# Performance work log

Measured on AMD Instinct MI355X. Metric: run time of the kernel, lower is better.

Reference implementation:

```python
import jax, jax.numpy as jnp
import numpy as np

N_NODES = 100000

def _graph_conv(x, src, dst, W, b, num_nodes):
    # DGL GraphConv, norm='both', edge_weight=None:
    # h = D_in^{-1/2} * A * (D_out^{-1/2} * x @ W) + b
    ones = jnp.ones(src.shape[0], dtype=x.dtype)
    out_deg = jax.ops.segment_sum(ones, src, num_segments=num_nodes)
    in_deg = jax.ops.segment_sum(ones, dst, num_segments=num_nodes)
    norm_src = jax.lax.rsqrt(jnp.clip(out_deg, 1.0))  # [N]
    norm_dst = jax.lax.rsqrt(jnp.clip(in_deg, 1.0))   # [N]
    h = (x * norm_src[:, None]) @ W                    # [N, out] (weight first: in>=out)
    msg = h[src]                                       # gather over edges [E, out]
    agg = jax.ops.segment_sum(msg, dst, num_segments=num_nodes)  # scatter-add [N, out]
    return agg * norm_dst[:, None] + b


def setup_inputs() -> dict:
    key = jax.random.key(0)
    k = jax.random.split(key, 8)
    N, F, H, C, E = N_NODES, 512, 16, 40, 3200000
    x = jax.random.normal(k[0], (N, F), dtype=jnp.float32)
    edge_src = jax.random.randint(k[1], (E,), 0, N, dtype=jnp.int32)
    edge_dst = jax.random.randint(k[2], (E,), 0, N, dtype=jnp.int32)
    # Glorot-style init for GraphConv weights, zero bias (DGL defaults)
    W1 = jax.random.normal(k[3], (F, H), dtype=jnp.float32) * (1.0 / np.sqrt(F))
    b1 = jnp.zeros((H,), dtype=jnp.float32)
    W2 = jax.random.normal(k[4], (H, C), dtype=jnp.float32) * (1.0 / np.sqrt(H))
    b2 = jnp.zeros((C,), dtype=jnp.float32)
    return {"x": x, "edge_src": edge_src, "edge_dst": edge_dst,
            "W1": W1, "b1": b1, "W2": W2, "b2": b2}


def reference(x, edge_src, edge_dst, W1, b1, W2, b2):
    h = _graph_conv(x, edge_src, edge_dst, W1, b1, N_NODES)
    h = jax.nn.relu(h)
    # dropout p=0.5 is identity in eval mode
    out = _graph_conv(h, edge_src, edge_dst, W2, b2, N_NODES)
    return out
```

## Files before the change

kernel.cpp:

```cpp
#include <hip/hip_runtime.h>

#define F_IN  512
#define H_DIM 16
#define C_OUT 40
#define NBLK_P 256

static inline size_t align_up(size_t x, size_t a) { return (x + a - 1) / a * a; }

__global__ __launch_bounds__(256) void k_pcount(const int* __restrict__ keys, int E,
        int chunk, int nbk, int* __restrict__ histT) {
    __shared__ int h[512];
    for (int i = threadIdx.x; i < nbk; i += 256) h[i] = 0;
    __syncthreads();
    int b = blockIdx.x;
    int s = b * chunk, e = min(s + chunk, E);
    for (int i = s + threadIdx.x; i < e; i += 256)
        atomicAdd(&h[keys[i] >> 8], 1);
    __syncthreads();
    for (int i = threadIdx.x; i < nbk; i += 256)
        histT[i * NBLK_P + b] = h[i];
}

__global__ void k_scan1(const int* __restrict__ in, int* __restrict__ out,
                        int* __restrict__ bsums, int n) {
    __shared__ int tmp[256];
    int t = threadIdx.x;
    int gid = blockIdx.x * 256 + t;
    int v = (gid < n) ? in[gid] : 0;
    tmp[t] = v;
    __syncthreads();
    for (int off = 1; off < 256; off <<= 1) {
        int add = (t >= off) ? tmp[t - off] : 0;
        __syncthreads();
        tmp[t] += add;
        __syncthreads();
    }
    if (gid < n) out[gid] = tmp[t] - v;
    if (t == 255) bsums[blockIdx.x] = tmp[255];
}

__global__ void k_scan2(int* bsums, int nb) {
    __shared__ int tmp[512];
    int t = threadIdx.x;
    int v = (t < nb) ? bsums[t] : 0;
    tmp[t] = v;
    __syncthreads();
    for (int off = 1; off < 512; off <<= 1) {
        int add = (t >= off) ? tmp[t - off] : 0;
        __syncthreads();
        tmp[t] += add;
        __syncthreads();
    }
    if (t < nb) bsums[t] = tmp[t] - v;
}

__global__ void k_scan3(int* __restrict__ out, const int* __restrict__ bsums, int n) {
    int gid = blockIdx.x * 256 + threadIdx.x;
    if (gid < n) out[gid] += bsums[blockIdx.x];
}

__global__ __launch_bounds__(256) void k_pscat_key(const int* __restrict__ keys, int E,
        int chunk, const int* __restrict__ histT, int* __restrict__ outk) {
    __shared__ int cnt[512];
    for (int i = threadIdx.x; i < 512; i += 256) cnt[i] = 0;
    __syncthreads();
    int b = blockIdx.x;
    int s = b * chunk, e = min(s + chunk, E);
    for (int i = s + threadIdx.x; i < e; i += 256) {
        int k = keys[i];
        int bk = k >> 8;
        int r = atomicAdd(&cnt[bk], 1);
        outk[histT[bk * NBLK_P + b] + r] = k;
    }
}

__global__ __launch_bounds__(256) void k_pscat_pair(const int* __restrict__ src,
        const int* __restrict__ dst, int E, int chunk,
        const int* __restrict__ histT, int2* __restrict__ outp) {
    __shared__ int cnt[512];
    for (int i = threadIdx.x; i < 512; i += 256) cnt[i] = 0;
    __syncthreads();
    int b = blockIdx.x;
    int s = b * chunk, e = min(s + chunk, E);
    for (int i = s + threadIdx.x; i < e; i += 256) {
        int d = dst[i];
        int bk = d >> 8;
        int r = atomicAdd(&cnt[bk], 1);
        outp[histT[bk * NBLK_P + b] + r] = make_int2(src[i], d);
    }
}

__global__ __launch_bounds__(256) void k_bcount(const int* __restrict__ keysb,
        const int* __restrict__ histT, int nbk, int E, int N, int* __restrict__ deg) {
    __shared__ int h[256];
    int t = threadIdx.x, b = blockIdx.x;
    int bstart = histT[b * NBLK_P];
    int bend = (b + 1 < nbk) ? histT[(b + 1) * NBLK_P] : E;
    h[t] = 0;
    __syncthreads();
    for (int i = bstart + t; i < bend; i += 256)
        atomicAdd(&h[keysb[i] & 255], 1);
    __syncthreads();
    int node = (b << 8) + t;
    if (node < N) deg[node] = h[t];
}

__global__ __launch_bounds__(256) void k_bbuild(const int2* __restrict__ pairsb,
        const int* __restrict__ histT, int nbk, int E, int N,
        int* __restrict__ indeg, int* __restrict__ csroff, int* __restrict__ csrsrc) {
    __shared__ int h[256], offs[256], cnt[256], tmp[256];
    int t = threadIdx.x, b = blockIdx.x;
    int bstart = histT[b * NBLK_P];
    int bend = (b + 1 < nbk) ? histT[(b + 1) * NBLK_P] : E;
    h[t] = 0; cnt[t] = 0;
    __syncthreads();
    for (int i = bstart + t; i < bend; i += 256)
        atomicAdd(&h[pairsb[i].y & 255], 1);
    __syncthreads();
    int v = h[t];
    tmp[t] = v;
    __syncthreads();
    for (int off = 1; off < 256; off <<= 1) {
        int add = (t >= off) ? tmp[t - off] : 0;
        __syncthreads();
        tmp[t] += add;
        __syncthreads();
    }
    offs[t] = tmp[t] - v;
    __syncthreads();
    int node = (b << 8) + t;
    if (node < N) {
        indeg[node] = v;
        csroff[node] = bstart + offs[t];
    }
    for (int i = bstart + t; i < bend; i += 256) {
        int2 p = pairsb[i];
        int l = p.y & 255;
        int r = atomicAdd(&cnt[l], 1);
        csrsrc[bstart + offs[l] + r] = p.x;
    }
}

__global__ __launch_bounds__(256) void k_gemm1(const float* __restrict__ x,
        const float* __restrict__ W1, const int* __restrict__ outdeg,
        float* __restrict__ h1, int n) {
    __shared__ float Ws[F_IN * H_DIM];
    for (int i = threadIdx.x; i < F_IN * H_DIM / 4; i += 256)
        ((float4*)Ws)[i] = ((const float4*)W1)[i];
    __syncthreads();

    int row = blockIdx.x * 256 + threadIdx.x;
    if (row >= n) return;
    const float4* xr = (const float4*)(x + (size_t)row * F_IN);

    float acc[H_DIM];
#pragma unroll
    for (int j = 0; j < H_DIM; ++j) acc[j] = 0.f;

    for (int c = 0; c < F_IN / 16; ++c) {
        float4 xv0 = xr[c * 4 + 0];
        float4 xv1 = xr[c * 4 + 1];
        float4 xv2 = xr[c * 4 + 2];
        float4 xv3 = xr[c * 4 + 3];
        float xs[16] = {xv0.x, xv0.y, xv0.z, xv0.w,
                        xv1.x, xv1.y, xv1.z, xv1.w,
                        xv2.x, xv2.y, xv2.z, xv2.w,
                        xv3.x, xv3.y, xv3.z, xv3.w};
#pragma unroll
        for (int kk = 0; kk < 16; ++kk) {
            const float* wr = &Ws[(c * 16 + kk) * H_DIM];
#pragma unroll
            for (int j = 0; j < H_DIM; ++j) acc[j] += xs[kk] * wr[j];
        }
    }

    float ns = rsqrtf(fmaxf((float)outdeg[row], 1.f));
    float4* o = (float4*)(h1 + (size_t)row * H_DIM);
#pragma unroll
    for (int qq = 0; qq < 4; ++qq)
        o[qq] = make_float4(acc[qq * 4 + 0] * ns, acc[qq * 4 + 1] * ns,
                            acc[qq * 4 + 2] * ns, acc[qq * 4 + 3] * ns);
}

__global__ __launch_bounds__(256) void k_agg1(const int* __restrict__ csroff,
        const int* __restrict__ indeg, const int* __restrict__ outdeg,
        const int* __restrict__ csrsrc, const float* __restrict__ h1,
        const float* __restrict__ b1, float* __restrict__ g, int n) {
    int t = threadIdx.x;
    int q = t & 3;
    int lv = t >> 2;
    int v = blockIdx.x * 64 + lv;
    if (v >= n) return;
    int start = csroff[v];
    int len = indeg[v];
    const float4* h4 = (const float4*)h1;
    float4 acc = make_float4(0.f, 0.f, 0.f, 0.f);
    for (int i = 0; i < len; ++i) {
        int s = csrsrc[start + i];
        float4 m = h4[(size_t)s * 4 + q];
        acc.x += m.x; acc.y += m.y; acc.z += m.z; acc.w += m.w;
    }
    float nd = rsqrtf(fmaxf((float)len, 1.f));
    float ns = rsqrtf(fmaxf((float)outdeg[v], 1.f));
    float4 bb = ((const float4*)b1)[q];
    float4 r;
    r.x = fmaxf(acc.x * nd + bb.x, 0.f) * ns;
    r.y = fmaxf(acc.y * nd + bb.y, 0.f) * ns;
    r.z = fmaxf(acc.z * nd + bb.z, 0.f) * ns;
    r.w = fmaxf(acc.w * nd + bb.w, 0.f) * ns;
    ((float4*)g)[(size_t)v * 4 + q] = r;
}

__global__ __launch_bounds__(256) void k_agg2(const int* __restrict__ csroff,
        const int* __restrict__ indeg, const int* __restrict__ csrsrc,
        const float* __restrict__ gbuf, const float* __restrict__ W2,
        const float* __restrict__ b2, float* __restrict__ out, int n) {
    __shared__ float Ws[H_DIM * C_OUT];
    __shared__ float agg[64][17];
    int t = threadIdx.x;
    for (int i = t; i < H_DIM * C_OUT; i += 256) Ws[i] = W2[i];

    int q = t & 3;
    int lv = t >> 2;
    int v = blockIdx.x * 64 + lv;
    float4 acc = make_float4(0.f, 0.f, 0.f, 0.f);
    if (v < n) {
        int start = csroff[v];
        int len = indeg[v];
        const float4* g4 = (const float4*)gbuf;
        for (int i = 0; i < len; ++i) {
            int s = csrsrc[start + i];
            float4 m = g4[(size_t)s * 4 + q];
            acc.x += m.x; acc.y += m.y; acc.z += m.z; acc.w += m.w;
        }
    }
    agg[lv][q * 4 + 0] = acc.x;
    agg[lv][q * 4 + 1] = acc.y;
    agg[lv][q * 4 + 2] = acc.z;
    agg[lv][q * 4 + 3] = acc.w;
    __syncthreads();

    for (int idx = t; idx < 64 * C_OUT; idx += 256) {
        int dlv = idx / C_OUT;
        int c = idx % C_OUT;
        int dv = blockIdx.x * 64 + dlv;
        if (dv < n) {
            float s = 0.f;
#pragma unroll
            for (int k = 0; k < H_DIM; ++k) s += agg[dlv][k] * Ws[k * C_OUT + c];
            float nd = rsqrtf(fmaxf((float)indeg[dv], 1.f));
            out[(size_t)dv * C_OUT + c] = s * nd + b2[c];
        }
    }
}

extern "C" void kernel_launch(void* const* d_in, const int* in_sizes, int n_in,
                              void* d_out, int out_size, void* d_ws, size_t ws_size,
                              hipStream_t stream) {
    const float* x  = (const float*)d_in[0];
    const int* esrc = (const int*)d_in[1];
    const int* edst = (const int*)d_in[2];
    const float* W1 = (const float*)d_in[3];
    const float* b1 = (const float*)d_in[4];
    const float* W2 = (const float*)d_in[5];
    const float* b2 = (const float*)d_in[6];
    float* out = (float*)d_out;

    const int N = in_sizes[0] / F_IN;
    const int E = in_sizes[1];
    const int nbk = (N + 255) >> 8;
    const int n2 = nbk * NBLK_P;
    const int chunk = (E + NBLK_P - 1) / NBLK_P;

    char* p = (char*)d_ws;
    auto alloc = [&](size_t bytes) -> char* {
        char* r = p; p += align_up(bytes, 256); return r;
    };
    int*  histS  = (int*)alloc((size_t)n2 * 4);
    int*  histT  = (int*)alloc((size_t)n2 * 4);
    int*  bsums  = (int*)alloc(512 * 4);
    int2* pairsb = (int2*)alloc((size_t)E * 8);
    int*  srcb   = (int*)alloc((size_t)E * 4);
    int*  indeg  = (int*)alloc((size_t)N * 4);
    int*  outdeg = (int*)alloc((size_t)N * 4);
    int*  csroff = (int*)alloc((size_t)N * 4);

    int*   csrsrc = srcb;
    float* h1     = (float*)pairsb;
    float* g      = h1 + (size_t)N * H_DIM;

    int nbs = (n2 + 255) / 256;

    k_pcount<<<NBLK_P, 256, 0, stream>>>(esrc, E, chunk, nbk, histS);
    k_scan1<<<nbs, 256, 0, stream>>>(histS, histS, bsums, n2);
    k_scan2<<<1, 512, 0, stream>>>(bsums, nbs);
    k_scan3<<<nbs, 256, 0, stream>>>(histS, bsums, n2);
    k_pscat_key<<<NBLK_P, 256, 0, stream>>>(esrc, E, chunk, histS, srcb);
    k_bcount<<<nbk, 256, 0, stream>>>(srcb, histS, nbk, E, N, outdeg);

    k_pcount<<<NBLK_P, 256, 0, stream>>>(edst, E, chunk, nbk, histT);
    k_scan1<<<nbs, 256, 0, stream>>>(histT, histT, bsums, n2);
    k_scan2<<<1, 512, 0, stream>>>(bsums, nbs);
    k_scan3<<<nbs, 256, 0, stream>>>(histT, bsums, n2);
    k_pscat_pair<<<NBLK_P, 256, 0, stream>>>(esrc, edst, E, chunk, histT, pairsb);
    k_bbuild<<<nbk, 256, 0, stream>>>(pairsb, histT, nbk, E, N, indeg, csroff, csrsrc);

    k_gemm1<<<(N + 255) / 256, 256, 0, stream>>>(x, W1, outdeg, h1, N);
    int nb64 = (N + 63) / 64;
    k_agg1<<<nb64, 256, 0, stream>>>(csroff, indeg, outdeg, csrsrc, h1, b1, g, N);
    k_agg2<<<nb64, 256, 0, stream>>>(csroff, indeg, csrsrc, g, W2, b2, out, N);
}
```

Before: 316.1 us.

## Fuse src/dst CSR build passes and pack bucketed edges into compact formats

```diff
diff --git a/kernel.cpp b/kernel.cpp
--- a/kernel.cpp
+++ b/kernel.cpp
@@ -7,115 +7,115 @@
 
 static inline size_t align_up(size_t x, size_t a) { return (x + a - 1) / a * a; }
 
-__global__ __launch_bounds__(256) void k_pcount(const int* __restrict__ keys, int E,
-        int chunk, int nbk, int* __restrict__ histT) {
-    __shared__ int h[512];
-    for (int i = threadIdx.x; i < nbk; i += 256) h[i] = 0;
-    __syncthreads();
-    int b = blockIdx.x;
-    int s = b * chunk, e = min(s + chunk, E);
-    for (int i = s + threadIdx.x; i < e; i += 256)
-        atomicAdd(&h[keys[i] >> 8], 1);
-    __syncthreads();
-    for (int i = threadIdx.x; i < nbk; i += 256)
-        histT[i * NBLK_P + b] = h[i];
-}
-
-__global__ void k_scan1(const int* __restrict__ in, int* __restrict__ out,
-                        int* __restrict__ bsums, int n) {
-    __shared__ int tmp[256];
-    int t = threadIdx.x;
-    int gid = blockIdx.x * 256 + t;
-    int v = (gid < n) ? in[gid] : 0;
-    tmp[t] = v;
-    __syncthreads();
-    for (int off = 1; off < 256; off <<= 1) {
-        int add = (t >= off) ? tmp[t - off] : 0;
-        __syncthreads();
-        tmp[t] += add;
-        __syncthreads();
-    }
-    if (gid < n) out[gid] = tmp[t] - v;
-    if (t == 255) bsums[blockIdx.x] = tmp[255];
-}
-
-__global__ void k_scan2(int* bsums, int nb) {
-    __shared__ int tmp[512];
-    int t = threadIdx.x;
-    int v = (t < nb) ? bsums[t] : 0;
-    tmp[t] = v;
-    __syncthreads();
-    for (int off = 1; off < 512; off <<= 1) {
-        int add = (t >= off) ? tmp[t - off] : 0;
-        __syncthreads();
-        tmp[t] += add;
-        __syncthreads();
-    }
-    if (t < nb) bsums[t] = tmp[t] - v;
-}
-
-__global__ void k_scan3(int* __restrict__ out, const int* __restrict__ bsums, int n) {
-    int gid = blockIdx.x * 256 + threadIdx.x;
-    if (gid < n) out[gid] += bsums[blockIdx.x];
-}
-
-__global__ __launch_bounds__(256) void k_pscat_key(const int* __restrict__ keys, int E,
-        int chunk, const int* __restrict__ histT, int* __restrict__ outk) {
-    __shared__ int cnt[512];
-    for (int i = threadIdx.x; i < 512; i += 256) cnt[i] = 0;
+__global__ __launch_bounds__(256) void k_pcount(const int* __restrict__ src,
+        const int* __restrict__ dst, int E, int chunk, int nbk,
+        int* __restrict__ histS, int* __restrict__ histT) {
+    __shared__ int hs[512], hd[512];
+    for (int i = threadIdx.x; i < 512; i += 256) { hs[i] = 0; hd[i] = 0; }
     __syncthreads();
     int b = blockIdx.x;
     int s = b * chunk, e = min(s + chunk, E);
     for (int i = s + threadIdx.x; i < e; i += 256) {
-        int k = keys[i];
-        int bk = k >> 8;
-        int r = atomicAdd(&cnt[bk], 1);
-        outk[histT[bk * NBLK_P + b] + r] = k;
-    }
-}
-
-__global__ __launch_bounds__(256) void k_pscat_pair(const int* __restrict__ src,
+        atomicAdd(&hs[src[i] >> 8], 1);
+        atomicAdd(&hd[dst[i] >> 8], 1);
+    }
+    __syncthreads();
+    for (int i = threadIdx.x; i < nbk; i += 256) {
+        histS[i * NBLK_P + b] = hs[i];
+        histT[i * NBLK_P + b] = hd[i];
+    }
+}
+
+__global__ void k_scan1(int* __restrict__ histS, int* __restrict__ histT,
+                        int* __restrict__ bsums) {
+    __shared__ int tmp[256];
+    int* h = blockIdx.y ? histT : histS;
+    int* bs = bsums + blockIdx.y * 512;
+    int t = threadIdx.x;
+    int gid = blockIdx.x * 256 + t;
+    int v = h[gid];
+    tmp[t] = v;
+    __syncthreads();
+    for (int off = 1; off < 256; off <<= 1) {
+        int add = (t >= off) ? tmp[t - off] : 0;
+        __syncthreads();
+        tmp[t] += add;
+        __syncthreads();
+    }
+    h[gid] = tmp[t] - v;
+    if (t == 255) bs[blockIdx.x] = tmp[255];
+}
+
+__global__ void k_scan2(int* __restrict__ bsums, int nb) {
+    __shared__ int tmp[512];
+    int* bs = bsums + blockIdx.x * 512;
+    int t = threadIdx.x;
+    int v = (t < nb) ? bs[t] : 0;
+    tmp[t] = v;
+    __syncthreads();
+    for (int off = 1; off < 512; off <<= 1) {
+        int add = (t >= off) ? tmp[t - off] : 0;
+        __syncthreads();
+        tmp[t] += add;
+        __syncthreads();
+    }
+    if (t < nb) bs[t] = tmp[t] - v;
+}
+
+__global__ void k_scan3(int* __restrict__ histS, int* __restrict__ histT,
+                        const int* __restrict__ bsums) {
+    int* h = blockIdx.y ? histT : histS;
+    const int* bs = bsums + blockIdx.y * 512;
+    h[blockIdx.x * 256 + threadIdx.x] += bs[blockIdx.x];
+}
+
+__global__ __launch_bounds__(256) void k_pscat(const int* __restrict__ src,
         const int* __restrict__ dst, int E, int chunk,
-        const int* __restrict__ histT, int2* __restrict__ outp) {
-    __shared__ int cnt[512];
-    for (int i = threadIdx.x; i < 512; i += 256) cnt[i] = 0;
+        const int* __restrict__ histS, const int* __restrict__ histT,
+        unsigned char* __restrict__ srcb, unsigned int* __restrict__ pairsb) {
+    __shared__ int cs[512], cd[512];
+    for (int i = threadIdx.x; i < 512; i += 256) { cs[i] = 0; cd[i] = 0; }
     __syncthreads();
     int b = blockIdx.x;
     int s = b * chunk, e = min(s + chunk, E);
     for (int i = s + threadIdx.x; i < e; i += 256) {
+        int k = src[i];
         int d = dst[i];
-        int bk = d >> 8;
-        int r = atomicAdd(&cnt[bk], 1);
-        outp[histT[bk * NBLK_P + b] + r] = make_int2(src[i], d);
-    }
-}
-
-__global__ __launch_bounds__(256) void k_bcount(const int* __restrict__ keysb,
-        const int* __restrict__ histT, int nbk, int E, int N, int* __restrict__ deg) {
-    __shared__ int h[256];
-    int t = threadIdx.x, b = blockIdx.x;
-    int bstart = histT[b * NBLK_P];
-    int bend = (b + 1 < nbk) ? histT[(b + 1) * NBLK_P] : E;
-    h[t] = 0;
-    __syncthreads();
-    for (int i = bstart + t; i < bend; i += 256)
-        atomicAdd(&h[keysb[i] & 255], 1);
-    __syncthreads();
-    int node = (b << 8) + t;
-    if (node < N) deg[node] = h[t];
-}
-
-__global__ __launch_bounds__(256) void k_bbuild(const int2* __restrict__ pairsb,
-        const int* __restrict__ histT, int nbk, int E, int N,
+        int bks = k >> 8;
+        int bkd = d >> 8;
+        int rs = atomicAdd(&cs[bks], 1);
+        int rd = atomicAdd(&cd[bkd], 1);
+        srcb[histS[bks * NBLK_P + b] + rs] = (unsigned char)(k & 255);
+        pairsb[histT[bkd * NBLK_P + b] + rd] =
+            (unsigned int)k | ((unsigned int)(d & 255) << 24);
+    }
+}
+
+__global__ __launch_bounds__(256) void k_bbuild(const unsigned char* __restrict__ srcb,
+        const unsigned int* __restrict__ pairsb,
+        const int* __restrict__ histS, const int* __restrict__ histT,
+        int nbk, int E, int N, int* __restrict__ outdeg,
         int* __restrict__ indeg, int* __restrict__ csroff, int* __restrict__ csrsrc) {
     __shared__ int h[256], offs[256], cnt[256], tmp[256];
     int t = threadIdx.x, b = blockIdx.x;
+    int node = (b << 8) + t;
+
+    int sstart = histS[b * NBLK_P];
+    int send = (b + 1 < nbk) ? histS[(b + 1) * NBLK_P] : E;
+    h[t] = 0;
+    __syncthreads();
+    for (int i = sstart + t; i < send; i += 256)
+        atomicAdd(&h[srcb[i]], 1);
+    __syncthreads();
+    if (node < N) outdeg[node] = h[t];
+    __syncthreads();
+
     int bstart = histT[b * NBLK_P];
     int bend = (b + 1 < nbk) ? histT[(b + 1) * NBLK_P] : E;
     h[t] = 0; cnt[t] = 0;
     __syncthreads();
     for (int i = bstart + t; i < bend; i += 256)
-        atomicAdd(&h[pairsb[i].y & 255], 1);
+        atomicAdd(&h[pairsb[i] >> 24], 1);
     __syncthreads();
     int v = h[t];
     tmp[t] = v;
@@ -128,16 +128,15 @@
     }
     offs[t] = tmp[t] - v;
     __syncthreads();
-    int node = (b << 8) + t;
     if (node < N) {
         indeg[node] = v;
         csroff[node] = bstart + offs[t];
     }
     for (int i = bstart + t; i < bend; i += 256) {
-        int2 p = pairsb[i];
-        int l = p.y & 255;
+        unsigned int p = pairsb[i];
+        int l = p >> 24;
         int r = atomicAdd(&cnt[l], 1);
-        csrsrc[bstart + offs[l] + r] = p.x;
+        csrsrc[bstart + offs[l] + r] = (int)(p & 0xFFFFFF);
     }
 }
 
@@ -152,6 +151,7 @@
     int row = blockIdx.x * 256 + threadIdx.x;
     if (row >= n) return;
     const float4* xr = (const float4*)(x + (size_t)row * F_IN);
+    float ns = rsqrtf(fmaxf((float)outdeg[row], 1.f));
 
     float acc[H_DIM];
 #pragma unroll
@@ -174,7 +174,6 @@
         }
     }
 
-    float ns = rsqrtf(fmaxf((float)outdeg[row], 1.f));
     float4* o = (float4*)(h1 + (size_t)row * H_DIM);
 #pragma unroll
     for (int qq = 0; qq < 4; ++qq)
@@ -195,7 +194,22 @@
     int len = indeg[v];
     const float4* h4 = (const float4*)h1;
     float4 acc = make_float4(0.f, 0.f, 0.f, 0.f);
-    for (int i = 0; i < len; ++i) {
+    int i = 0;
+    for (; i + 4 <= len; i += 4) {
+        int s0 = csrsrc[start + i + 0];
+        int s1 = csrsrc[start + i + 1];
+        int s2 = csrsrc[start + i + 2];
+        int s3 = csrsrc[start + i + 3];
+        float4 m0 = h4[(size_t)s0 * 4 + q];
+        float4 m1 = h4[(size_t)s1 * 4 + q];
+        float4 m2 = h4[(size_t)s2 * 4 + q];
+        float4 m3 = h4[(size_t)s3 * 4 + q];
+        acc.x += m0.x + m1.x + m2.x + m3.x;
+        acc.y += m0.y + m1.y + m2.y + m3.y;
+        acc.z += m0.z + m1.z + m2.z + m3.z;
+        acc.w += m0.w + m1.w + m2.w + m3.w;
+    }
+    for (; i < len; ++i) {
         int s = csrsrc[start + i];
         float4 m = h4[(size_t)s * 4 + q];
         acc.x += m.x; acc.y += m.y; acc.z += m.z; acc.w += m.w;
@@ -228,7 +242,22 @@
         int start = csroff[v];
         int len = indeg[v];
         const float4* g4 = (const float4*)gbuf;
-        for (int i = 0; i < len; ++i) {
+        int i = 0;
+        for (; i + 4 <= len; i += 4) {
+            int s0 = csrsrc[start + i + 0];
+            int s1 = csrsrc[start + i + 1];
+            int s2 = csrsrc[start + i + 2];
+            int s3 = csrsrc[start + i + 3];
+            float4 m0 = g4[(size_t)s0 * 4 + q];
+            float4 m1 = g4[(size_t)s1 * 4 + q];
+            float4 m2 = g4[(size_t)s2 * 4 + q];
+            float4 m3 = g4[(size_t)s3 * 4 + q];
+            acc.x += m0.x + m1.x + m2.x + m3.x;
+            acc.y += m0.y + m1.y + m2.y + m3.y;
+            acc.z += m0.z + m1.z + m2.z + m3.z;
+            acc.w += m0.w + m1.w + m2.w + m3.w;
+        }
+        for (; i < len; ++i) {
             int s = csrsrc[start + i];
             float4 m = g4[(size_t)s * 4 + q];
             acc.x += m.x; acc.y += m.y; acc.z += m.z; acc.w += m.w;
@@ -269,41 +298,33 @@
     const int N = in_sizes[0] / F_IN;
     const int E = in_sizes[1];
     const int nbk = (N + 255) >> 8;
-    const int n2 = nbk * NBLK_P;
     const int chunk = (E + NBLK_P - 1) / NBLK_P;
 
     char* p = (char*)d_ws;
     auto alloc = [&](size_t bytes) -> char* {
         char* r = p; p += align_up(bytes, 256); return r;
     };
-    int*  histS  = (int*)alloc((size_t)n2 * 4);
-    int*  histT  = (int*)alloc((size_t)n2 * 4);
-    int*  bsums  = (int*)alloc(512 * 4);
-    int2* pairsb = (int2*)alloc((size_t)E * 8);
-    int*  srcb   = (int*)alloc((size_t)E * 4);
+    int*  histS  = (int*)alloc((size_t)nbk * NBLK_P * 4);
+    int*  histT  = (int*)alloc((size_t)nbk * NBLK_P * 4);
+    int*  bsums  = (int*)alloc(1024 * 4);
+    unsigned int*  pairsb = (unsigned int*)alloc((size_t)E * 4);
+    unsigned char* srcb   = (unsigned char*)alloc((size_t)E);
+    int*  csrsrc = (int*)alloc((size_t)E * 4);
     int*  indeg  = (int*)alloc((size_t)N * 4);
     int*  outdeg = (int*)alloc((size_t)N * 4);
     int*  csroff = (int*)alloc((size_t)N * 4);
 
-    int*   csrsrc = srcb;
-    float* h1     = (float*)pairsb;
-    float* g      = h1 + (size_t)N * H_DIM;
-
-    int nbs = (n2 + 255) / 256;
-
-    k_pcount<<<NBLK_P, 256, 0, stream>>>(esrc, E, chunk, nbk, histS);
-    k_scan1<<<nbs, 256, 0, stream>>>(histS, histS, bsums, n2);
-    k_scan2<<<1, 512, 0, stream>>>(bsums, nbs);
-    k_scan3<<<nbs, 256, 0, stream>>>(histS, bsums, n2);
-    k_pscat_key<<<NBLK_P, 256, 0, stream>>>(esrc, E, chunk, histS, srcb);
-    k_bcount<<<nbk, 256, 0, stream>>>(srcb, histS, nbk, E, N, outdeg);
-
-    k_pcount<<<NBLK_P, 256, 0, stream>>>(edst, E, chunk, nbk, histT);
-    k_scan1<<<nbs, 256, 0, stream>>>(histT, histT, bsums, n2);
-    k_scan2<<<1, 512, 0, stream>>>(bsums, nbs);
-    k_scan3<<<nbs, 256, 0, stream>>>(histT, bsums, n2);
-    k_pscat_pair<<<NBLK_P, 256, 0, stream>>>(esrc, edst, E, chunk, histT, pairsb);
-    k_bbuild<<<nbk, 256, 0, stream>>>(pairsb, histT, nbk, E, N, indeg, csroff, csrsrc);
+    float* h1 = (float*)pairsb;
+    float* g  = h1 + (size_t)N * H_DIM;
+
+    k_pcount<<<NBLK_P, 256, 0, stream>>>(esrc, edst, E, chunk, nbk, histS, histT);
+    k_scan1<<<dim3(nbk, 2), 256, 0, stream>>>(histS, histT, bsums);
+    k_scan2<<<2, 512, 0, stream>>>(bsums, nbk);
+    k_scan3<<<dim3(nbk, 2), 256, 0, stream>>>(histS, histT, bsums);
+    k_pscat<<<NBLK_P, 256, 0, stream>>>(esrc, edst, E, chunk, histS, histT,
+                                        srcb, pairsb);
+    k_bbuild<<<nbk, 256, 0, stream>>>(srcb, pairsb, histS, histT, nbk, E, N,
+                                      outdeg, indeg, csroff, csrsrc);
 
     k_gemm1<<<(N + 255) / 256, 256, 0, stream>>>(x, W1, outdeg, h1, N);
     int nb64 = (N + 63) / 64;
```

Result: faster. 279.6 us (-11.6%).
